# Kernel tuning notes

Measured on AMD Instinct MI355X. Metric: run time of the kernel, lower is better.

## Reference

```python
import jax, jax.numpy as jnp
import numpy as np

N = 50000
E = 600000
D = 128        # in_dim == hidden_dim
L = 3          # num_layers
BN_EPS = 1e-5


def setup_inputs() -> dict:
    key = jax.random.key(0)
    ks = jax.random.split(key, 12)
    x = jax.random.normal(ks[0], (N, D), dtype=jnp.float32)
    edge_index = jax.random.randint(ks[1], (2, E), 0, N, dtype=jnp.int64)
    s = 1.0 / np.sqrt(D)
    # SAGEConv per layer: out = lin_l(mean_aggr(x_src)) + lin_r(x_root); bias on lin_l only
    Wl = jax.random.uniform(ks[2], (L, D, D), jnp.float32, -s, s)
    Wr = jax.random.uniform(ks[3], (L, D, D), jnp.float32, -s, s)
    bl = jax.random.uniform(ks[4], (L, D), jnp.float32, -s, s)
    gamma = jnp.ones((L, D), jnp.float32)
    beta = jnp.zeros((L, D), jnp.float32)
    h = D // 2
    s2 = 1.0 / np.sqrt(h)
    W1 = jax.random.uniform(ks[5], (D, h), jnp.float32, -s, s)
    b1 = jax.random.uniform(ks[6], (h,), jnp.float32, -s, s)
    W2 = jax.random.uniform(ks[7], (h, 2), jnp.float32, -s2, s2)
    b2 = jax.random.uniform(ks[8], (2,), jnp.float32, -s2, s2)
    return {"x": x, "edge_index": edge_index, "Wl": Wl, "Wr": Wr, "bl": bl,
            "gamma": gamma, "beta": beta, "W1": W1, "b1": b1, "W2": W2, "b2": b2}


def _sage_layer(x, src, dst, Wl, Wr, bl):
    # mean aggregation of source features into destination nodes
    msg = x[src]                                            # [E, D] gather
    summed = jax.ops.segment_sum(msg, dst, num_segments=N)  # [N, D]
    cnt = jax.ops.segment_sum(jnp.ones((E,), x.dtype), dst, num_segments=N)
    mean = summed / jnp.maximum(cnt, 1.0)[:, None]
    return mean @ Wl + bl + x @ Wr


def _bn(x, gamma, beta):
    mu = jnp.mean(x, axis=0)
    var = jnp.mean(jnp.square(x - mu), axis=0)  # biased var (torch BN)
    return (x - mu) * (gamma / jnp.sqrt(var + BN_EPS)) + beta


def reference(x, edge_index, Wl, Wr, bl, gamma, beta, W1, b1, W2, b2):
    src, dst = edge_index[0], edge_index[1]
    h = x
    for i in range(L):
        h = _sage_layer(h, src, dst, Wl[i], Wr[i], bl[i])
        h = _bn(h, gamma[i], beta[i])
        h = jax.nn.relu(h)
        # dropout: identity at inference
    z = jax.nn.relu(h @ W1 + b1)
    logits = z @ W2 + b2
    return logits, jax.nn.softmax(logits, axis=-1)
```

## Files before the change

kernel.cpp:

```cpp
#include <hip/hip_runtime.h>
#include <math.h>

#define N_NODES 50000
#define N_EDGES 600000
#define D 128
#define NLAYERS 3
#define BN_EPS 1e-5f
#define NBLK ((N_NODES + 255) / 256)
#define GBLK ((N_NODES + 63) / 64)
#define NW (NLAYERS * 128 * 256)

typedef short short8 __attribute__((ext_vector_type(8)));
typedef float f32x4 __attribute__((ext_vector_type(4)));

__device__ __forceinline__ float b2f(unsigned short u) {
    return __uint_as_float(((unsigned int)u) << 16);
}
__device__ __forceinline__ unsigned short f2b(float f) {
    unsigned int b = __float_as_uint(f);
    return (unsigned short)((b + 0x7fffu + ((b >> 16) & 1u)) >> 16);
}

__global__ void k_cvt_x(const float* __restrict__ x, unsigned short* __restrict__ xb) {
    int idx = blockIdx.x * 256 + threadIdx.x;
    if (idx >= N_NODES * D / 4) return;
    float4 v = ((const float4*)x)[idx];
    ushort4 o;
    o.x = f2b(v.x); o.y = f2b(v.y); o.z = f2b(v.z); o.w = f2b(v.w);
    ((ushort4*)xb)[idx] = o;
}

__global__ void k_cvt_weights(const float* __restrict__ Wl, const float* __restrict__ Wr,
                              const float* __restrict__ W1, unsigned short* __restrict__ Wt,
                              unsigned short* __restrict__ W1t) {
    int idx = blockIdx.x * 256 + threadIdx.x;
    if (idx < NW) {
        int l = idx >> 15;
        int rem = idx & 32767;
        int c = rem >> 8;
        int k = rem & 255;
        float v = (k < 128) ? Wl[l * 16384 + k * 128 + c]
                            : Wr[l * 16384 + (k - 128) * 128 + c];
        Wt[idx] = f2b(v);
    } else {
        int i = idx - NW;
        if (i < 64 * 128) {
            int c = i >> 7;
            int k = i & 127;
            W1t[i] = f2b(W1[k * 64 + c]);
        }
    }
}

__global__ void k_hist(const int* __restrict__ dst, int* __restrict__ cnt) {
    int e = blockIdx.x * blockDim.x + threadIdx.x;
    if (e < N_EDGES) atomicAdd(&cnt[dst[e]], 1);
}

__global__ void k_local_scan(const int* __restrict__ cnt, int* __restrict__ row_ptr,
                             int* __restrict__ bsum) {
    __shared__ int sm[256];
    int tid = threadIdx.x;
    int i = blockIdx.x * 256 + tid;
    int v = (i < N_NODES) ? cnt[i] : 0;
    sm[tid] = v;
    __syncthreads();
    for (int off = 1; off < 256; off <<= 1) {
        int t = (tid >= off) ? sm[tid - off] : 0;
        __syncthreads();
        sm[tid] += t;
        __syncthreads();
    }
    int incl = sm[tid];
    if (i < N_NODES) row_ptr[i] = incl - v;
    if (tid == 255) bsum[blockIdx.x] = incl;
}

__global__ void k_scan_bsums(const int* __restrict__ bsum, int* __restrict__ boff,
                             int* __restrict__ row_ptr) {
    __shared__ int sm[256];
    int tid = threadIdx.x;
    int v = (tid < NBLK) ? bsum[tid] : 0;
    sm[tid] = v;
    __syncthreads();
    for (int off = 1; off < 256; off <<= 1) {
        int t = (tid >= off) ? sm[tid - off] : 0;
        __syncthreads();
        sm[tid] += t;
        __syncthreads();
    }
    int incl = sm[tid];
    if (tid < NBLK) boff[tid] = incl - v;
    if (tid == 255) row_ptr[N_NODES] = incl;
}

__global__ void k_add_off(int* __restrict__ row_ptr, const int* __restrict__ boff,
                          int* __restrict__ row_fill) {
    int i = blockIdx.x * 256 + threadIdx.x;
    if (i < N_NODES) {
        int v = row_ptr[i] + boff[i >> 8];
        row_ptr[i] = v;
        row_fill[i] = v;
    }
}

__global__ void k_fill(const int* __restrict__ src, const int* __restrict__ dst,
                       int* __restrict__ row_fill, int* __restrict__ edge_sorted) {
    int e = blockIdx.x * blockDim.x + threadIdx.x;
    if (e < N_EDGES) {
        int pos = atomicAdd(&row_fill[dst[e]], 1);
        edge_sorted[pos] = src[e];
    }
}

__global__ __launch_bounds__(256) void k_agg(const unsigned short* __restrict__ h,
                                             const int* __restrict__ edge_sorted,
                                             const int* __restrict__ row_ptr,
                                             unsigned short* __restrict__ meanbuf) {
    int node = blockIdx.x * 16 + (threadIdx.x >> 4);
    int lane = threadIdx.x & 15;
    int beg = row_ptr[node], end = row_ptr[node + 1];
    const short8* hp = (const short8*)h;
    float a[8];
#pragma unroll
    for (int i = 0; i < 8; ++i) a[i] = 0.f;
    int e1 = end - 1;
    for (int j = beg; j < end; j += 4) {
        int j1 = j + 1, j2 = j + 2, j3 = j + 3;
        int i1 = (j1 <= e1) ? j1 : e1;
        int i2 = (j2 <= e1) ? j2 : e1;
        int i3 = (j3 <= e1) ? j3 : e1;
        int s0 = edge_sorted[j];
        int s1 = edge_sorted[i1];
        int s2 = edge_sorted[i2];
        int s3 = edge_sorted[i3];
        short8 v0 = hp[(size_t)s0 * 16 + lane];
        short8 v1 = hp[(size_t)s1 * 16 + lane];
        short8 v2 = hp[(size_t)s2 * 16 + lane];
        short8 v3 = hp[(size_t)s3 * 16 + lane];
        float m1 = (j1 < end) ? 1.f : 0.f;
        float m2 = (j2 < end) ? 1.f : 0.f;
        float m3 = (j3 < end) ? 1.f : 0.f;
#pragma unroll
        for (int i = 0; i < 8; ++i) {
            float t = a[i] + b2f((unsigned short)v0[i]);
            t = fmaf(m1, b2f((unsigned short)v1[i]), t);
            t = fmaf(m2, b2f((unsigned short)v2[i]), t);
            t = fmaf(m3, b2f((unsigned short)v3[i]), t);
            a[i] = t;
        }
    }
    float inv = 1.0f / fmaxf((float)(end - beg), 1.0f);
    short8 o;
#pragma unroll
    for (int i = 0; i < 8; ++i) o[i] = (short)f2b(a[i] * inv);
    ((short8*)meanbuf)[(size_t)node * 16 + lane] = o;
}

__global__ __launch_bounds__(256) void k_gemm_mfma(const unsigned short* __restrict__ Am,
                                                   const unsigned short* __restrict__ Ah,
                                                   const unsigned short* __restrict__ Wt,
                                                   const float* __restrict__ bias,
                                                   float* __restrict__ pre,
                                                   float* __restrict__ partial) {
    __shared__ float red[4][256];
    int wave = threadIdx.x >> 6;
    int lane = threadIdx.x & 63;
    int col = lane & 15;
    int quad = lane >> 4;
    int row_base = blockIdx.x * 64 + wave * 16;
    bool valid = row_base < N_NODES;

    f32x4 acc[8];
#pragma unroll
    for (int t = 0; t < 8; ++t) acc[t] = (f32x4){0.f, 0.f, 0.f, 0.f};

    if (valid) {
        int arow = row_base + col;
#pragma unroll
        for (int kk = 0; kk < 8; ++kk) {
            const unsigned short* Aptr = (kk < 4) ? Am : Ah;
            int kofs = (kk & 3) * 32 + quad * 8;
            short8 a = *(const short8*)(Aptr + (size_t)arow * D + kofs);
#pragma unroll
            for (int t = 0; t < 8; ++t) {
                short8 b = *(const short8*)(Wt + (size_t)(t * 16 + col) * 256 + kk * 32 + quad * 8);
                acc[t] = __builtin_amdgcn_mfma_f32_16x16x32_bf16(a, b, acc[t], 0, 0, 0);
            }
        }
    }

#pragma unroll
    for (int t = 0; t < 8; ++t) {
        float s = 0.f, ss = 0.f;
        if (valid) {
            float bc = bias[t * 16 + col];
#pragma unroll
            for (int r = 0; r < 4; ++r) {
                float v = acc[t][r] + bc;
                pre[(size_t)(row_base + quad * 4 + r) * D + t * 16 + col] = v;
                s += v;
                ss += v * v;
            }
        }
        s += __shfl_xor(s, 16);  ss += __shfl_xor(ss, 16);
        s += __shfl_xor(s, 32);  ss += __shfl_xor(ss, 32);
        if (quad == 0) {
            red[wave][t * 16 + col] = s;
            red[wave][128 + t * 16 + col] = ss;
        }
    }
    __syncthreads();
    int tid = threadIdx.x;
    partial[(size_t)blockIdx.x * 256 + tid] =
        red[0][tid] + red[1][tid] + red[2][tid] + red[3][tid];
}

__global__ void k_reduce_stats(const float* __restrict__ partial, float* __restrict__ sums) {
    int t = threadIdx.x;
    float a0 = 0.f, a1 = 0.f, a2 = 0.f, a3 = 0.f;
    int b = 0;
    for (; b + 4 <= GBLK; b += 4) {
        a0 += partial[(size_t)(b + 0) * 256 + t];
        a1 += partial[(size_t)(b + 1) * 256 + t];
        a2 += partial[(size_t)(b + 2) * 256 + t];
        a3 += partial[(size_t)(b + 3) * 256 + t];
    }
    for (; b < GBLK; ++b) a0 += partial[(size_t)b * 256 + t];
    sums[t] = (a0 + a1) + (a2 + a3);
}

__global__ void k_bnrelu(const float* __restrict__ pre, const float* __restrict__ sums,
                         const float* __restrict__ sumsq, const float* __restrict__ gamma,
                         const float* __restrict__ beta, unsigned short* __restrict__ outbuf) {
    int idx = blockIdx.x * blockDim.x + threadIdx.x;
    const int total = N_NODES * D / 4;
    if (idx >= total) return;
    int col4 = (idx & 31) * 4;
    float4 v = ((const float4*)pre)[idx];
    float vv[4] = {v.x, v.y, v.z, v.w};
    unsigned short o[4];
    const float invN = 1.0f / (float)N_NODES;
#pragma unroll
    for (int c = 0; c < 4; ++c) {
        int j = col4 + c;
        float mu  = sums[j] * invN;
        float var = sumsq[j] * invN - mu * mu;
        float sc = gamma[j] * rsqrtf(var + BN_EPS);
        float sh = beta[j] - mu * sc;
        float x = vv[c] * sc + sh;
        o[c] = f2b(fmaxf(x, 0.f));
    }
    ushort4 ov; ov.x = o[0]; ov.y = o[1]; ov.z = o[2]; ov.w = o[3];
    ((ushort4*)outbuf)[idx] = ov;
}

__global__ __launch_bounds__(256) void k_mlp_mfma(const unsigned short* __restrict__ h,
                                                  const unsigned short* __restrict__ W1t,
                                                  const float* __restrict__ b1,
                                                  const float* __restrict__ W2,
                                                  const float* __restrict__ b2,
                                                  float* __restrict__ out) {
    int wave = threadIdx.x >> 6;
    int lane = threadIdx.x & 63;
    int col = lane & 15;
    int quad = lane >> 4;
    int row_base = blockIdx.x * 64 + wave * 16;
    if (row_base >= N_NODES) return;
    int arow = row_base + col;

    f32x4 acc[4];
#pragma unroll
    for (int t = 0; t < 4; ++t) acc[t] = (f32x4){0.f, 0.f, 0.f, 0.f};

#pragma unroll
    for (int kk = 0; kk < 4; ++kk) {
        short8 a = *(const short8*)(h + (size_t)arow * D + kk * 32 + quad * 8);
#pragma unroll
        for (int t = 0; t < 4; ++t) {
            short8 b = *(const short8*)(W1t + (size_t)(t * 16 + col) * 128 + kk * 32 + quad * 8);
            acc[t] = __builtin_amdgcn_mfma_f32_16x16x32_bf16(a, b, acc[t], 0, 0, 0);
        }
    }

    float pa[4] = {0.f, 0.f, 0.f, 0.f}, pb[4] = {0.f, 0.f, 0.f, 0.f};
#pragma unroll
    for (int t = 0; t < 4; ++t) {
        int c = t * 16 + col;
        float bb = b1[c];
        float w2a = W2[c * 2], w2b = W2[c * 2 + 1];
#pragma unroll
        for (int r = 0; r < 4; ++r) {
            float z = fmaxf(acc[t][r] + bb, 0.f);
            pa[r] = fmaf(z, w2a, pa[r]);
            pb[r] = fmaf(z, w2b, pb[r]);
        }
    }
#pragma unroll
    for (int m = 1; m < 16; m <<= 1) {
#pragma unroll
        for (int r = 0; r < 4; ++r) {
            pa[r] += __shfl_xor(pa[r], m);
            pb[r] += __shfl_xor(pb[r], m);
        }
    }
    if (col < 4) {
        int node = row_base + quad * 4 + col;
        float l0 = pa[col] + b2[0], l1 = pb[col] + b2[1];
        float2 lg; lg.x = l0; lg.y = l1;
        ((float2*)out)[node] = lg;
        float m = fmaxf(l0, l1);
        float e0 = expf(l0 - m), e1 = expf(l1 - m);
        float s = 1.0f / (e0 + e1);
        float2 pr; pr.x = e0 * s; pr.y = e1 * s;
        ((float2*)(out + 2 * N_NODES))[node] = pr;
    }
}

extern "C" void kernel_launch(void* const* d_in, const int* in_sizes, int n_in,
                              void* d_out, int out_size, void* d_ws, size_t ws_size,
                              hipStream_t stream) {
    const float* x     = (const float*)d_in[0];
    const int*   ei    = (const int*)d_in[1];
    const int*   src   = ei;
    const int*   dst   = ei + N_EDGES;
    const float* Wl    = (const float*)d_in[2];
    const float* Wr    = (const float*)d_in[3];
    const float* bl    = (const float*)d_in[4];
    const float* gamma = (const float*)d_in[5];
    const float* beta  = (const float*)d_in[6];
    const float* W1    = (const float*)d_in[7];
    const float* b1    = (const float*)d_in[8];
    const float* W2    = (const float*)d_in[9];
    const float* b2    = (const float*)d_in[10];
    float* out = (float*)d_out;

    char* ws = (char*)d_ws;
    size_t off = 0;
    auto alloc = [&](size_t bytes) -> void* {
        void* p = ws + off;
        off += (bytes + 255) & ~(size_t)255;
        return p;
    };
    unsigned short* xb   = (unsigned short*)alloc((size_t)N_NODES * D * 2);
    unsigned short* Ha   = (unsigned short*)alloc((size_t)N_NODES * D * 2);
    unsigned short* Mb   = (unsigned short*)alloc((size_t)N_NODES * D * 2);
    float* pre           = (float*)alloc((size_t)N_NODES * D * 4);
    unsigned short* Wtb  = (unsigned short*)alloc((size_t)NW * 2);
    unsigned short* W1t  = (unsigned short*)alloc((size_t)64 * 128 * 2);
    float* partial       = (float*)alloc((size_t)GBLK * 256 * 4);
    int* cnt             = (int*)alloc((size_t)N_NODES * 4);
    int* row_ptr         = (int*)alloc((size_t)(N_NODES + 1) * 4);
    int* row_fill        = (int*)alloc((size_t)N_NODES * 4);
    int* edge_sorted     = (int*)alloc((size_t)N_EDGES * 4);
    int* bsum            = (int*)alloc((size_t)NBLK * 4);
    int* boff            = (int*)alloc((size_t)NBLK * 4);
    float* sums          = (float*)alloc(256 * 4);
    float* sumsq = sums + 128;

    k_cvt_x<<<(N_NODES * D / 4 + 255) / 256, 256, 0, stream>>>(x, xb);
    k_cvt_weights<<<(NW + 64 * 128 + 255) / 256, 256, 0, stream>>>(Wl, Wr, W1, Wtb, W1t);

    hipMemsetAsync(cnt, 0, (size_t)N_NODES * 4, stream);
    k_hist<<<(N_EDGES + 255) / 256, 256, 0, stream>>>(dst, cnt);
    k_local_scan<<<NBLK, 256, 0, stream>>>(cnt, row_ptr, bsum);
    k_scan_bsums<<<1, 256, 0, stream>>>(bsum, boff, row_ptr);
    k_add_off<<<NBLK, 256, 0, stream>>>(row_ptr, boff, row_fill);
    k_fill<<<(N_EDGES + 255) / 256, 256, 0, stream>>>(src, dst, row_fill, edge_sorted);

    const unsigned short* hcur = xb;
    unsigned short* hout[3] = {Ha, xb, Ha};
    for (int l = 0; l < NLAYERS; ++l) {
        k_agg<<<N_NODES / 16, 256, 0, stream>>>(hcur, edge_sorted, row_ptr, Mb);
        k_gemm_mfma<<<GBLK, 256, 0, stream>>>(Mb, hcur, Wtb + (size_t)l * 32768,
                                              bl + l * D, pre, partial);
        k_reduce_stats<<<1, 256, 0, stream>>>(partial, sums);
        k_bnrelu<<<(N_NODES * D / 4 + 255) / 256, 256, 0, stream>>>(
            pre, sums, sumsq, gamma + l * D, beta + l * D, hout[l]);
        hcur = hout[l];
    }

    k_mlp_mfma<<<GBLK, 256, 0, stream>>>(hcur, W1t, b1, W2, b2, out);
}
```

Baseline: 426.3 us.

## Fuse neighbor aggregation into SAGE GEMM via LDS and atomic BN stats

Merges the mean-aggregation kernel into the MFMA GEMM kernel. Each 64-row block gathers its neighbor means into shared memory, which removes the global round trip of the mean buffer. The separate stats-reduction kernel is replaced by per-block atomicAdd into per-layer sums that are zeroed once up front. Two launches per layer disappear, but the fused kernel has only 782 blocks doing irregular gathers, so latency hiding for the gather phase may drop.

```diff
diff --git a/kernel.cpp b/kernel.cpp
--- a/kernel.cpp
+++ b/kernel.cpp
@@ -9,6 +9,7 @@
 #define NBLK ((N_NODES + 255) / 256)
 #define GBLK ((N_NODES + 63) / 64)
 #define NW (NLAYERS * 128 * 256)
+#define MPAD 136
 
 typedef short short8 __attribute__((ext_vector_type(8)));
 typedef float f32x4 __attribute__((ext_vector_type(4)));
@@ -113,62 +114,73 @@
     }
 }
 
-__global__ __launch_bounds__(256) void k_agg(const unsigned short* __restrict__ h,
-                                             const int* __restrict__ edge_sorted,
-                                             const int* __restrict__ row_ptr,
-                                             unsigned short* __restrict__ meanbuf) {
-    int node = blockIdx.x * 16 + (threadIdx.x >> 4);
-    int lane = threadIdx.x & 15;
-    int beg = row_ptr[node], end = row_ptr[node + 1];
-    const short8* hp = (const short8*)h;
-    float a[8];
-#pragma unroll
-    for (int i = 0; i < 8; ++i) a[i] = 0.f;
-    int e1 = end - 1;
-    for (int j = beg; j < end; j += 4) {
-        int j1 = j + 1, j2 = j + 2, j3 = j + 3;
-        int i1 = (j1 <= e1) ? j1 : e1;
-        int i2 = (j2 <= e1) ? j2 : e1;
-        int i3 = (j3 <= e1) ? j3 : e1;
-        int s0 = edge_sorted[j];
-        int s1 = edge_sorted[i1];
-        int s2 = edge_sorted[i2];
-        int s3 = edge_sorted[i3];
-        short8 v0 = hp[(size_t)s0 * 16 + lane];
-        short8 v1 = hp[(size_t)s1 * 16 + lane];
-        short8 v2 = hp[(size_t)s2 * 16 + lane];
-        short8 v3 = hp[(size_t)s3 * 16 + lane];
-        float m1 = (j1 < end) ? 1.f : 0.f;
-        float m2 = (j2 < end) ? 1.f : 0.f;
-        float m3 = (j3 < end) ? 1.f : 0.f;
-#pragma unroll
-        for (int i = 0; i < 8; ++i) {
-            float t = a[i] + b2f((unsigned short)v0[i]);
-            t = fmaf(m1, b2f((unsigned short)v1[i]), t);
-            t = fmaf(m2, b2f((unsigned short)v2[i]), t);
-            t = fmaf(m3, b2f((unsigned short)v3[i]), t);
-            a[i] = t;
-        }
-    }
-    float inv = 1.0f / fmaxf((float)(end - beg), 1.0f);
-    short8 o;
-#pragma unroll
-    for (int i = 0; i < 8; ++i) o[i] = (short)f2b(a[i] * inv);
-    ((short8*)meanbuf)[(size_t)node * 16 + lane] = o;
-}
-
-__global__ __launch_bounds__(256) void k_gemm_mfma(const unsigned short* __restrict__ Am,
-                                                   const unsigned short* __restrict__ Ah,
-                                                   const unsigned short* __restrict__ Wt,
-                                                   const float* __restrict__ bias,
-                                                   float* __restrict__ pre,
-                                                   float* __restrict__ partial) {
+__global__ __launch_bounds__(256) void k_layer(const unsigned short* __restrict__ h,
+                                               const int* __restrict__ edge_sorted,
+                                               const int* __restrict__ row_ptr,
+                                               const unsigned short* __restrict__ Wt,
+                                               const float* __restrict__ bias,
+                                               float* __restrict__ pre,
+                                               float* __restrict__ sums) {
+    __shared__ unsigned short meanb[64][MPAD];
     __shared__ float red[4][256];
-    int wave = threadIdx.x >> 6;
-    int lane = threadIdx.x & 63;
+
+    int tid = threadIdx.x;
+    int row0 = blockIdx.x * 64;
+
+    {
+        int sub = tid >> 4;
+        int lane = tid & 15;
+        const short8* hp = (const short8*)h;
+#pragma unroll
+        for (int p = 0; p < 4; ++p) {
+            int nl = p * 16 + sub;
+            int node = row0 + nl;
+            if (node < N_NODES) {
+                int beg = row_ptr[node], end = row_ptr[node + 1];
+                float a[8];
+#pragma unroll
+                for (int i = 0; i < 8; ++i) a[i] = 0.f;
+                int e1 = end - 1;
+                for (int j = beg; j < end; j += 4) {
+                    int j1 = j + 1, j2 = j + 2, j3 = j + 3;
+                    int i1 = (j1 <= e1) ? j1 : e1;
+                    int i2 = (j2 <= e1) ? j2 : e1;
+                    int i3 = (j3 <= e1) ? j3 : e1;
+                    int s0 = edge_sorted[j];
+                    int s1 = edge_sorted[i1];
+                    int s2 = edge_sorted[i2];
+                    int s3 = edge_sorted[i3];
+                    short8 v0 = hp[(size_t)s0 * 16 + lane];
+                    short8 v1 = hp[(size_t)s1 * 16 + lane];
+                    short8 v2 = hp[(size_t)s2 * 16 + lane];
+                    short8 v3 = hp[(size_t)s3 * 16 + lane];
+                    float m1 = (j1 < end) ? 1.f : 0.f;
+                    float m2 = (j2 < end) ? 1.f : 0.f;
+                    float m3 = (j3 < end) ? 1.f : 0.f;
+#pragma unroll
+                    for (int i = 0; i < 8; ++i) {
+                        float t = a[i] + b2f((unsigned short)v0[i]);
+                        t = fmaf(m1, b2f((unsigned short)v1[i]), t);
+                        t = fmaf(m2, b2f((unsigned short)v2[i]), t);
+                        t = fmaf(m3, b2f((unsigned short)v3[i]), t);
+                        a[i] = t;
+                    }
+                }
+                float inv = 1.0f / fmaxf((float)(end - beg), 1.0f);
+                short8 o;
+#pragma unroll
+                for (int i = 0; i < 8; ++i) o[i] = (short)f2b(a[i] * inv);
+                *(short8*)&meanb[nl][lane * 8] = o;
+            }
+        }
+    }
+    __syncthreads();
+
+    int wave = tid >> 6;
+    int lane = tid & 63;
     int col = lane & 15;
     int quad = lane >> 4;
-    int row_base = blockIdx.x * 64 + wave * 16;
+    int row_base = row0 + wave * 16;
     bool valid = row_base < N_NODES;
 
     f32x4 acc[8];
@@ -176,12 +188,16 @@
     for (int t = 0; t < 8; ++t) acc[t] = (f32x4){0.f, 0.f, 0.f, 0.f};
 
     if (valid) {
-        int arow = row_base + col;
+        int arow_l = wave * 16 + col;
+        int arow_g = row_base + col;
 #pragma unroll
         for (int kk = 0; kk < 8; ++kk) {
-            const unsigned short* Aptr = (kk < 4) ? Am : Ah;
-            int kofs = (kk & 3) * 32 + quad * 8;
-            short8 a = *(const short8*)(Aptr + (size_t)arow * D + kofs);
+            short8 a;
+            if (kk < 4) {
+                a = *(const short8*)&meanb[arow_l][kk * 32 + quad * 8];
+            } else {
+                a = *(const short8*)(h + (size_t)arow_g * D + (kk - 4) * 32 + quad * 8);
+            }
 #pragma unroll
             for (int t = 0; t < 8; ++t) {
                 short8 b = *(const short8*)(Wt + (size_t)(t * 16 + col) * 256 + kk * 32 + quad * 8);
@@ -211,31 +227,17 @@
         }
     }
     __syncthreads();
-    int tid = threadIdx.x;
-    partial[(size_t)blockIdx.x * 256 + tid] =
-        red[0][tid] + red[1][tid] + red[2][tid] + red[3][tid];
-}
-
-__global__ void k_reduce_stats(const float* __restrict__ partial, float* __restrict__ sums) {
-    int t = threadIdx.x;
-    float a0 = 0.f, a1 = 0.f, a2 = 0.f, a3 = 0.f;
-    int b = 0;
-    for (; b + 4 <= GBLK; b += 4) {
-        a0 += partial[(size_t)(b + 0) * 256 + t];
-        a1 += partial[(size_t)(b + 1) * 256 + t];
-        a2 += partial[(size_t)(b + 2) * 256 + t];
-        a3 += partial[(size_t)(b + 3) * 256 + t];
-    }
-    for (; b < GBLK; ++b) a0 += partial[(size_t)b * 256 + t];
-    sums[t] = (a0 + a1) + (a2 + a3);
+    float pv = red[0][tid] + red[1][tid] + red[2][tid] + red[3][tid];
+    atomicAdd(&sums[tid], pv);
 }
 
 __global__ void k_bnrelu(const float* __restrict__ pre, const float* __restrict__ sums,
-                         const float* __restrict__ sumsq, const float* __restrict__ gamma,
-                         const float* __restrict__ beta, unsigned short* __restrict__ outbuf) {
+                         const float* __restrict__ gamma, const float* __restrict__ beta,
+                         unsigned short* __restrict__ outbuf) {
     int idx = blockIdx.x * blockDim.x + threadIdx.x;
     const int total = N_NODES * D / 4;
     if (idx >= total) return;
+    const float* sumsq = sums + 128;
     int col4 = (idx & 31) * 4;
     float4 v = ((const float4*)pre)[idx];
     float vv[4] = {v.x, v.y, v.z, v.w};
@@ -344,19 +346,16 @@
     };
     unsigned short* xb   = (unsigned short*)alloc((size_t)N_NODES * D * 2);
     unsigned short* Ha   = (unsigned short*)alloc((size_t)N_NODES * D * 2);
-    unsigned short* Mb   = (unsigned short*)alloc((size_t)N_NODES * D * 2);
     float* pre           = (float*)alloc((size_t)N_NODES * D * 4);
     unsigned short* Wtb  = (unsigned short*)alloc((size_t)NW * 2);
     unsigned short* W1t  = (unsigned short*)alloc((size_t)64 * 128 * 2);
-    float* partial       = (float*)alloc((size_t)GBLK * 256 * 4);
     int* cnt             = (int*)alloc((size_t)N_NODES * 4);
     int* row_ptr         = (int*)alloc((size_t)(N_NODES + 1) * 4);
     int* row_fill        = (int*)alloc((size_t)N_NODES * 4);
     int* edge_sorted     = (int*)alloc((size_t)N_EDGES * 4);
     int* bsum            = (int*)alloc((size_t)NBLK * 4);
     int* boff            = (int*)alloc((size_t)NBLK * 4);
-    float* sums          = (float*)alloc(256 * 4);
-    float* sumsq = sums + 128;
+    float* sums_all      = (float*)alloc(NLAYERS * 256 * 4);
 
     k_cvt_x<<<(N_NODES * D / 4 + 255) / 256, 256, 0, stream>>>(x, xb);
     k_cvt_weights<<<(NW + 64 * 128 + 255) / 256, 256, 0, stream>>>(Wl, Wr, W1, Wtb, W1t);
@@ -368,15 +367,16 @@
     k_add_off<<<NBLK, 256, 0, stream>>>(row_ptr, boff, row_fill);
     k_fill<<<(N_EDGES + 255) / 256, 256, 0, stream>>>(src, dst, row_fill, edge_sorted);
 
+    hipMemsetAsync(sums_all, 0, NLAYERS * 256 * 4, stream);
+
     const unsigned short* hcur = xb;
     unsigned short* hout[3] = {Ha, xb, Ha};
     for (int l = 0; l < NLAYERS; ++l) {
-        k_agg<<<N_NODES / 16, 256, 0, stream>>>(hcur, edge_sorted, row_ptr, Mb);
-        k_gemm_mfma<<<GBLK, 256, 0, stream>>>(Mb, hcur, Wtb + (size_t)l * 32768,
-                                              bl + l * D, pre, partial);
-        k_reduce_stats<<<1, 256, 0, stream>>>(partial, sums);
+        float* sums = sums_all + l * 256;
+        k_layer<<<GBLK, 256, 0, stream>>>(hcur, edge_sorted, row_ptr,
+                                          Wtb + (size_t)l * 32768, bl + l * D, pre, sums);
         k_bnrelu<<<(N_NODES * D / 4 + 255) / 256, 256, 0, stream>>>(
-            pre, sums, sumsq, gamma + l * D, beta + l * D, hout[l]);
+            pre, sums, gamma + l * D, beta + l * D, hout[l]);
         hcur = hout[l];
     }
 
```

New measurement: 387.7 us. 1.1x faster.
